# Optimization experiments

Hardware: AMD Instinct MI355X
Metric: run time of the kernel (lower is better)

## Reference

```python
import jax, jax.numpy as jnp
import numpy as np

D = 768
H = 12
DH = D // H  # 64


def setup_inputs() -> dict:
    key = jax.random.key(0)
    ks = jax.random.split(key, 7)
    B, N = 16, 1024
    sequences = jax.random.normal(ks[0], (B, N, D), dtype=jnp.float32)
    s = 1.0 / np.sqrt(DH)
    # per-head torch Linear params: weight [out, in] = [DH, DH], bias [DH]
    Wq = jax.random.uniform(ks[1], (H, DH, DH), jnp.float32, -s, s)
    Wk = jax.random.uniform(ks[2], (H, DH, DH), jnp.float32, -s, s)
    Wv = jax.random.uniform(ks[3], (H, DH, DH), jnp.float32, -s, s)
    bq = jax.random.uniform(ks[4], (H, DH), jnp.float32, -s, s)
    bk = jax.random.uniform(ks[5], (H, DH), jnp.float32, -s, s)
    bv = jax.random.uniform(ks[6], (H, DH), jnp.float32, -s, s)
    return {"sequences": sequences, "Wq": Wq, "Wk": Wk, "Wv": Wv,
            "bq": bq, "bk": bk, "bv": bv}


def reference(sequences, Wq, Wk, Wv, bq, bk, bv):
    B, N, _ = sequences.shape
    x = sequences.reshape(B, N, H, DH)  # head slices of the feature dim
    # torch Linear: y = x @ W.T + b  -> einsum over the 'in' axis of W
    q = jnp.einsum('bnhd,hed->bnhe', x, Wq) + bq
    k = jnp.einsum('bnhd,hed->bnhe', x, Wk) + bk
    v = jnp.einsum('bnhd,hed->bnhe', x, Wv) + bv
    scores = jnp.einsum('bnhe,bmhe->bhnm', q, k) / jnp.sqrt(jnp.float32(DH))
    attn = jax.nn.softmax(scores, axis=-1)  # [B,H,N,N]
    out = jnp.einsum('bhnm,bmhe->bnhe', attn, v)
    return out.reshape(B, N, H * DH)  # hstack of per-head outputs
```

## Files before the change

kernel.cpp:

```cpp
#include <hip/hip_runtime.h>


#define NH 12
#define DHEAD 64
#define BB 16
#define NSEQ 1024
#define DMODEL 768
#define LSTR 72
#define QSCALE 0.18033688f

typedef unsigned short u16;
typedef unsigned int u32;
typedef u16 u16x8 __attribute__((ext_vector_type(8)));
typedef u16 u16x4 __attribute__((ext_vector_type(4)));
typedef __bf16 bf16x8 __attribute__((ext_vector_type(8)));
typedef float f32x4 __attribute__((ext_vector_type(4)));
typedef int i32x2 __attribute__((ext_vector_type(2)));

union Frag { u16x8 u; bf16x8 b; u32 w[4]; };

__device__ __forceinline__ float fast_exp2(float x) {
#if __has_builtin(__builtin_amdgcn_exp2f)
    return __builtin_amdgcn_exp2f(x);
#else
    return exp2f(x);
#endif
}

__device__ __forceinline__ u16 f2bf(float f) {
    union { __bf16 h; u16 u; } c; c.h = (__bf16)f; return c.u;
}

__device__ __forceinline__ u32 pk2(float lo, float hi) {
    return (u32)f2bf(lo) | ((u32)f2bf(hi) << 16);
}

__device__ __forceinline__ u16x8 cvt8(const float* __restrict__ p) {
    f32x4 a = *(const f32x4*)p;
    f32x4 b = *(const f32x4*)(p + 4);
    Frag r;
    r.b[0] = (__bf16)a[0]; r.b[1] = (__bf16)a[1]; r.b[2] = (__bf16)a[2]; r.b[3] = (__bf16)a[3];
    r.b[4] = (__bf16)b[0]; r.b[5] = (__bf16)b[1]; r.b[6] = (__bf16)b[2]; r.b[7] = (__bf16)b[3];
    return r.u;
}

__device__ __forceinline__ int sw(int row, int slot) {
    return (row << 6) + (((slot + row) & 7) << 3);
}

__device__ __forceinline__ void lane4_shuffle(u32 a0, u32 a1, u32& wlo, u32& whi) {
    i32x2 t = __builtin_amdgcn_permlane32_swap((int)a0, (int)a1, false, false);
    i32x2 r = __builtin_amdgcn_permlane16_swap(t[0], t[1], false, false);
    wlo = (u32)r[0]; whi = (u32)r[1];
}

__global__ __launch_bounds__(256) void wcvt_kernel(
    const float* __restrict__ Wq, const float* __restrict__ Wk,
    const float* __restrict__ Wv, u16* __restrict__ Wb)
{
    const int bx = blockIdx.x;
    const int m = bx / 24;
    const int off = (bx % 24) * 2048 + threadIdx.x * 8;
    const float* srcs[3] = { Wq, Wk, Wv };
    *(u16x8*)(Wb + m * 49152 + off) = cvt8(srcs[m] + off);
}

__global__ __launch_bounds__(256) void kv_kernel(
    const float* __restrict__ x,
    const u16*  __restrict__ Wb,
    const float* __restrict__ bk, const float* __restrict__ bv,
    u16* __restrict__ Ko,
    u16* __restrict__ Vt)
{
    __shared__ __align__(16) u16 w_lds[2][64 * LSTR];
    __shared__ __align__(16) u16 x_lds[128 * LSTR];

    const int bid = blockIdx.x;
    const int h     = bid % NH;
    const int chunk = (bid / NH) & 7;
    const int b     = bid / (NH * 8);

    const int t = threadIdx.x, lane = t & 63, wave = t >> 6;
    const int qd = lane >> 4, lm = lane & 15;

    {
        const int row = t >> 2, d0 = (t & 3) * 16;
#pragma unroll
        for (int m = 0; m < 2; m++) {
            const u16* s = Wb + (1 + m) * 49152 + h * 4096 + row * 64 + d0;
            *(u16x8*)&w_lds[m][row * LSTR + d0]     = *(const u16x8*)s;
            *(u16x8*)&w_lds[m][row * LSTR + d0 + 8] = *(const u16x8*)(s + 8);
        }
        const int xr = t >> 1, xd = (t & 1) * 32;
        const float* s = x + ((size_t)(b * NSEQ + chunk * 128 + xr)) * DMODEL + h * DHEAD + xd;
#pragma unroll
        for (int i = 0; i < 4; i++)
            *(u16x8*)&x_lds[xr * LSTR + xd + i * 8] = cvt8(s + i * 8);
    }
    __syncthreads();

    Frag xfrag[2][2];
#pragma unroll
    for (int mt = 0; mt < 2; mt++)
#pragma unroll
        for (int kk = 0; kk < 2; kk++)
            xfrag[mt][kk].u = *(const u16x8*)&x_lds[(wave * 32 + mt * 16 + lm) * LSTR + kk * 32 + qd * 8];

    u16* tx = &x_lds[wave * 32 * LSTR];
    const int key_base = chunk * 128 + wave * 32;

#pragma unroll
    for (int et = 0; et < 4; et++) {
        Frag wfrag[2];
#pragma unroll
        for (int kk = 0; kk < 2; kk++)
            wfrag[kk].u = *(const u16x8*)&w_lds[0][(et * 16 + lm) * LSTR + kk * 32 + qd * 8];
        f32x4 acc0 = {0.f,0.f,0.f,0.f}, acc1 = {0.f,0.f,0.f,0.f};
#pragma unroll
        for (int kk = 0; kk < 2; kk++) {
            acc0 = __builtin_amdgcn_mfma_f32_16x16x32_bf16(wfrag[kk].b, xfrag[0][kk].b, acc0, 0, 0, 0);
            acc1 = __builtin_amdgcn_mfma_f32_16x16x32_bf16(wfrag[kk].b, xfrag[1][kk].b, acc1, 0, 0, 0);
        }
        f32x4 b4 = *(const f32x4*)&bk[h * DHEAD + et * 16 + qd * 4];
        u16x4 o0, o1;
#pragma unroll
        for (int r = 0; r < 4; r++) {
            o0[r] = f2bf(acc0[r] + b4[r]);
            o1[r] = f2bf(acc1[r] + b4[r]);
        }
        *(u16x4*)&tx[lm * LSTR + et * 16 + qd * 4]        = o0;
        *(u16x4*)&tx[(16 + lm) * LSTR + et * 16 + qd * 4] = o1;
    }
    {
        const size_t base_out = ((size_t)(b * NH + h) * NSEQ + key_base) * DHEAD;
#pragma unroll
        for (int j = 0; j < 4; j++) {
            const int row = j * 8 + (lane >> 3), col = (lane & 7) * 8;
            u16x8 v = *(const u16x8*)&tx[row * LSTR + col];
            *(u16x8*)(Ko + base_out + (size_t)row * DHEAD + col) = v;
        }
    }

    const size_t vt_base = ((size_t)(b * NH + h)) * DHEAD * NSEQ;
#pragma unroll
    for (int et = 0; et < 4; et++) {
        Frag wvfrag[2];
#pragma unroll
        for (int kk = 0; kk < 2; kk++)
            wvfrag[kk].u = *(const u16x8*)&w_lds[1][(et * 16 + lm) * LSTR + kk * 32 + qd * 8];
        const float bvv = bv[h * DHEAD + et * 16 + lm];
#pragma unroll
        for (int mt = 0; mt < 2; mt++) {
            f32x4 acc = {0.f,0.f,0.f,0.f};
#pragma unroll
            for (int kk = 0; kk < 2; kk++)
                acc = __builtin_amdgcn_mfma_f32_16x16x32_bf16(xfrag[mt][kk].b, wvfrag[kk].b, acc, 0, 0, 0);
            u16x4 o;
#pragma unroll
            for (int r = 0; r < 4; r++) o[r] = f2bf(acc[r] + bvv);
            *(u16x4*)(Vt + vt_base + (size_t)(et * 16 + lm) * NSEQ + key_base + mt * 16 + qd * 4) = o;
        }
    }
}

__global__ __launch_bounds__(256, 2) void attn_kernel(
    const float* __restrict__ x, const u16* __restrict__ Wb,
    const float* __restrict__ bq,
    const u16* __restrict__ K, const u16* __restrict__ Vt,
    float* __restrict__ out)
{
    __shared__ __align__(16) u16 k_lds[2][64 * 64];
    __shared__ __align__(16) u16 v_lds[2][64 * 64];

    const int bid = blockIdx.x;
    const int bh = bid % 192;
    const int qt = bid / 192;
    const int h = bh % NH, b = bh / NH;

    const int t = threadIdx.x, lane = t & 63, wave = t >> 6;
    const int qd = lane >> 4, lm = lane & 15;
    const size_t bh_off = (size_t)bh * NSEQ * DHEAD;
    const int tb = qt * 256;

    const u16* kb = K  + bh_off;
    const u16* vb = Vt + bh_off;

    const int srow = t >> 2, sc = t & 3;

    {
        const u16* wq = Wb + h * 4096 + srow * 64 + sc * 16;
        *(u16x8*)&k_lds[0][sw(srow, sc * 2)]     = *(const u16x8*)wq;
        *(u16x8*)&k_lds[0][sw(srow, sc * 2 + 1)] = *(const u16x8*)(wq + 8);
    }

    u16x8 kreg0, kreg1, vreg0, vreg1;
    {
        const u16* sk = kb + (size_t)srow * DHEAD + sc * 16;
        kreg0 = *(const u16x8*)sk; kreg1 = *(const u16x8*)(sk + 8);
        const u16* sv = vb + (size_t)srow * NSEQ + sc * 16;
        vreg0 = *(const u16x8*)sv; vreg1 = *(const u16x8*)(sv + 8);
    }
    __syncthreads();

    Frag qfrag[4][2];
#pragma unroll
    for (int mtl = 0; mtl < 4; mtl++) {
        const float* xs = x + ((size_t)(b * NSEQ + tb + wave * 64 + mtl * 16 + lm)) * DMODEL
                          + h * DHEAD + qd * 8;
        Frag xB[2];
        xB[0].u = cvt8(xs);
        xB[1].u = cvt8(xs + 32);
        u32 Ap[4], Bp[4];
#pragma unroll
        for (int et = 0; et < 4; et++) {
            Frag wqA[2];
#pragma unroll
            for (int kk = 0; kk < 2; kk++)
                wqA[kk].u = *(const u16x8*)&k_lds[0][sw(et * 16 + lm, kk * 4 + qd)];
            f32x4 acc = {0.f,0.f,0.f,0.f};
#pragma unroll
            for (int kk = 0; kk < 2; kk++)
                acc = __builtin_amdgcn_mfma_f32_16x16x32_bf16(wqA[kk].b, xB[kk].b, acc, 0, 0, 0);
            f32x4 b4 = *(const f32x4*)&bq[h * DHEAD + et * 16 + qd * 4];
            Ap[et] = pk2((acc[0] + b4[0]) * QSCALE, (acc[1] + b4[1]) * QSCALE);
            Bp[et] = pk2((acc[2] + b4[2]) * QSCALE, (acc[3] + b4[3]) * QSCALE);
        }
#pragma unroll
        for (int kk = 0; kk < 2; kk++) {
            lane4_shuffle(Ap[2 * kk], Ap[2 * kk + 1], qfrag[mtl][kk].w[0], qfrag[mtl][kk].w[2]);
            lane4_shuffle(Bp[2 * kk], Bp[2 * kk + 1], qfrag[mtl][kk].w[1], qfrag[mtl][kk].w[3]);
        }
    }

    *(u16x8*)&k_lds[1][sw(srow, sc * 2)]     = kreg0;
    *(u16x8*)&k_lds[1][sw(srow, sc * 2 + 1)] = kreg1;
    *(u16x8*)&v_lds[1][sw(srow, sc * 2)]     = vreg0;
    *(u16x8*)&v_lds[1][sw(srow, sc * 2 + 1)] = vreg1;
    {
        const u16* sk = kb + (size_t)(64 + srow) * DHEAD + sc * 16;
        kreg0 = *(const u16x8*)sk; kreg1 = *(const u16x8*)(sk + 8);
        const u16* sv = vb + (size_t)srow * NSEQ + 64 + sc * 16;
        vreg0 = *(const u16x8*)sv; vreg1 = *(const u16x8*)(sv + 8);
    }
    __syncthreads();

    f32x4 o_acc[4][4] = {};
    f32x4 rsum = {0.f, 0.f, 0.f, 0.f};

#pragma unroll 1
    for (int it = 0; it < NSEQ / 64; it++) {
        const int cur = 1 - (it & 1);

        Frag kfrag[4][2];
#pragma unroll
        for (int kt = 0; kt < 4; kt++)
#pragma unroll
            for (int kk = 0; kk < 2; kk++)
                kfrag[kt][kk].u = *(const u16x8*)&k_lds[cur][sw(kt * 16 + lm, kk * 4 + qd)];

        Frag pfrag[4][2];
#pragma unroll
        for (int mt = 0; mt < 4; mt++) {
            f32x4 st[4];
#pragma unroll
            for (int kt = 0; kt < 4; kt++) {
                f32x4 a = {0.f,0.f,0.f,0.f};
#pragma unroll
                for (int kk = 0; kk < 2; kk++)
                    a = __builtin_amdgcn_mfma_f32_16x16x32_bf16(kfrag[kt][kk].b, qfrag[mt][kk].b, a, 0, 0, 0);
                st[kt] = a;
            }
            float rs = 0.f;
            u32 Ap[4], Bp[4];
#pragma unroll
            for (int kt = 0; kt < 4; kt++) {
                float e0 = fast_exp2(st[kt][0]);
                float e1 = fast_exp2(st[kt][1]);
                float e2 = fast_exp2(st[kt][2]);
                float e3 = fast_exp2(st[kt][3]);
                rs += (e0 + e1) + (e2 + e3);
                Ap[kt] = pk2(e0, e1); Bp[kt] = pk2(e2, e3);
            }
            rsum[mt] += rs;
#pragma unroll
            for (int kk = 0; kk < 2; kk++) {
                lane4_shuffle(Ap[2 * kk], Ap[2 * kk + 1], pfrag[mt][kk].w[0], pfrag[mt][kk].w[2]);
                lane4_shuffle(Bp[2 * kk], Bp[2 * kk + 1], pfrag[mt][kk].w[1], pfrag[mt][kk].w[3]);
            }
        }

#pragma unroll
        for (int dt = 0; dt < 4; dt++) {
            Frag vfrag[2];
#pragma unroll
            for (int kk = 0; kk < 2; kk++)
                vfrag[kk].u = *(const u16x8*)&v_lds[cur][sw(dt * 16 + lm, kk * 4 + qd)];
#pragma unroll
            for (int kk = 0; kk < 2; kk++)
#pragma unroll
                for (int mt = 0; mt < 4; mt++)
                    o_acc[mt][dt] = __builtin_amdgcn_mfma_f32_16x16x32_bf16(pfrag[mt][kk].b, vfrag[kk].b, o_acc[mt][dt], 0, 0, 0);
        }

        if (it < NSEQ / 64 - 1) {
            *(u16x8*)&k_lds[1 - cur][sw(srow, sc * 2)]     = kreg0;
            *(u16x8*)&k_lds[1 - cur][sw(srow, sc * 2 + 1)] = kreg1;
            *(u16x8*)&v_lds[1 - cur][sw(srow, sc * 2)]     = vreg0;
            *(u16x8*)&v_lds[1 - cur][sw(srow, sc * 2 + 1)] = vreg1;
        }
        if (it < NSEQ / 64 - 2) {
            const u16* sk = kb + (size_t)((it + 2) * 64 + srow) * DHEAD + sc * 16;
            kreg0 = *(const u16x8*)sk; kreg1 = *(const u16x8*)(sk + 8);
            const u16* sv = vb + (size_t)srow * NSEQ + (it + 2) * 64 + sc * 16;
            vreg0 = *(const u16x8*)sv; vreg1 = *(const u16x8*)(sv + 8);
        }
        __syncthreads();
    }

#pragma unroll
    for (int mt = 0; mt < 4; mt++) {
        float s = rsum[mt];
        s += __shfl_xor(s, 16);
        s += __shfl_xor(s, 32);
        float inv = 1.f / s;
        float inv4[4];
#pragma unroll
        for (int r = 0; r < 4; r++) inv4[r] = __shfl(inv, qd * 4 + r);
#pragma unroll
        for (int dt = 0; dt < 4; dt++) {
            const int e = dt * 16 + lm;
#pragma unroll
            for (int r = 0; r < 4; r++) {
                const int n_tok = tb + wave * 64 + mt * 16 + qd * 4 + r;
                out[((size_t)(b * NSEQ + n_tok)) * DMODEL + h * DHEAD + e] =
                    o_acc[mt][dt][r] * inv4[r];
            }
        }
    }
}

extern "C" void kernel_launch(void* const* d_in, const int* in_sizes, int n_in,
                              void* d_out, int out_size, void* d_ws, size_t ws_size,
                              hipStream_t stream) {
    const float* x  = (const float*)d_in[0];
    const float* Wq = (const float*)d_in[1];
    const float* Wk = (const float*)d_in[2];
    const float* Wv = (const float*)d_in[3];
    const float* bq = (const float*)d_in[4];
    const float* bk = (const float*)d_in[5];
    const float* bv = (const float*)d_in[6];
    float* out = (float*)d_out;

    const size_t KV_ELEMS = (size_t)BB * NH * NSEQ * DHEAD;
    u16* Kw  = (u16*)d_ws;
    u16* Vtw = Kw + KV_ELEMS;
    u16* Wb  = Vtw + KV_ELEMS;

    wcvt_kernel<<<72, 256, 0, stream>>>(Wq, Wk, Wv, Wb);
    kv_kernel<<<BB * 8 * NH, 256, 0, stream>>>(x, Wb, bk, bv, Kw, Vtw);
    attn_kernel<<<(NSEQ / 256) * BB * NH, 256, 0, stream>>>(x, Wb, bq, Kw, Vtw, out);
}
```

Measured before the change: 99.13 us.

## Software-pipeline QK and PV MFMAs per query tile with setprio and higher occupancy

Restructures the attention inner loop so the QK^T scores for the next query sub-tile are issued while the exp/pack/shuffle of the current one runs, and the PV MFMAs are applied per sub-tile instead of after all four. V fragments are hoisted to registers once per iteration, and s_setprio raises wave priority around MFMA bursts. It also raises launch bounds to 3 blocks per CU and uses a packed bf16x2 conversion. The aim is to overlap transcendental/VALU work with matrix-core work. The cost is more live registers under a tighter occupancy bound, which risks spilling.

```diff
diff --git a/kernel.cpp b/kernel.cpp
--- a/kernel.cpp
+++ b/kernel.cpp
@@ -14,6 +14,7 @@
 typedef u16 u16x8 __attribute__((ext_vector_type(8)));
 typedef u16 u16x4 __attribute__((ext_vector_type(4)));
 typedef __bf16 bf16x8 __attribute__((ext_vector_type(8)));
+typedef __bf16 bf16x2 __attribute__((ext_vector_type(2)));
 typedef float f32x4 __attribute__((ext_vector_type(4)));
 typedef int i32x2 __attribute__((ext_vector_type(2)));
 
@@ -32,7 +33,9 @@
 }
 
 __device__ __forceinline__ u32 pk2(float lo, float hi) {
-    return (u32)f2bf(lo) | ((u32)f2bf(hi) << 16);
+    union { bf16x2 b; u32 u; } c;
+    c.b[0] = (__bf16)lo; c.b[1] = (__bf16)hi;
+    return c.u;
 }
 
 __device__ __forceinline__ u16x8 cvt8(const float* __restrict__ p) {
@@ -163,7 +166,7 @@
     }
 }
 
-__global__ __launch_bounds__(256, 2) void attn_kernel(
+__global__ __launch_bounds__(256, 3) void attn_kernel(
     const float* __restrict__ x, const u16* __restrict__ Wb,
     const float* __restrict__ bq,
     const u16* __restrict__ K, const u16* __restrict__ Vt,
@@ -257,19 +260,39 @@
 #pragma unroll
             for (int kk = 0; kk < 2; kk++)
                 kfrag[kt][kk].u = *(const u16x8*)&k_lds[cur][sw(kt * 16 + lm, kk * 4 + qd)];
-
-        Frag pfrag[4][2];
+        Frag vfrag[4][2];
+#pragma unroll
+        for (int dt = 0; dt < 4; dt++)
+#pragma unroll
+            for (int kk = 0; kk < 2; kk++)
+                vfrag[dt][kk].u = *(const u16x8*)&v_lds[cur][sw(dt * 16 + lm, kk * 4 + qd)];
+
+        f32x4 st[4];
+        __builtin_amdgcn_s_setprio(1);
+#pragma unroll
+        for (int kt = 0; kt < 4; kt++) {
+            f32x4 a = {0.f,0.f,0.f,0.f};
+            a = __builtin_amdgcn_mfma_f32_16x16x32_bf16(kfrag[kt][0].b, qfrag[0][0].b, a, 0, 0, 0);
+            a = __builtin_amdgcn_mfma_f32_16x16x32_bf16(kfrag[kt][1].b, qfrag[0][1].b, a, 0, 0, 0);
+            st[kt] = a;
+        }
+        __builtin_amdgcn_s_setprio(0);
+
 #pragma unroll
         for (int mt = 0; mt < 4; mt++) {
-            f32x4 st[4];
-#pragma unroll
-            for (int kt = 0; kt < 4; kt++) {
-                f32x4 a = {0.f,0.f,0.f,0.f};
-#pragma unroll
-                for (int kk = 0; kk < 2; kk++)
-                    a = __builtin_amdgcn_mfma_f32_16x16x32_bf16(kfrag[kt][kk].b, qfrag[mt][kk].b, a, 0, 0, 0);
-                st[kt] = a;
-            }
+            f32x4 stn[4];
+            if (mt < 3) {
+                __builtin_amdgcn_s_setprio(1);
+#pragma unroll
+                for (int kt = 0; kt < 4; kt++) {
+                    f32x4 a = {0.f,0.f,0.f,0.f};
+                    a = __builtin_amdgcn_mfma_f32_16x16x32_bf16(kfrag[kt][0].b, qfrag[mt + 1][0].b, a, 0, 0, 0);
+                    a = __builtin_amdgcn_mfma_f32_16x16x32_bf16(kfrag[kt][1].b, qfrag[mt + 1][1].b, a, 0, 0, 0);
+                    stn[kt] = a;
+                }
+                __builtin_amdgcn_s_setprio(0);
+            }
+
             float rs = 0.f;
             u32 Ap[4], Bp[4];
 #pragma unroll
@@ -282,24 +305,25 @@
                 Ap[kt] = pk2(e0, e1); Bp[kt] = pk2(e2, e3);
             }
             rsum[mt] += rs;
+            Frag pfrag[2];
 #pragma unroll
             for (int kk = 0; kk < 2; kk++) {
-                lane4_shuffle(Ap[2 * kk], Ap[2 * kk + 1], pfrag[mt][kk].w[0], pfrag[mt][kk].w[2]);
-                lane4_shuffle(Bp[2 * kk], Bp[2 * kk + 1], pfrag[mt][kk].w[1], pfrag[mt][kk].w[3]);
-            }
-        }
-
-#pragma unroll
-        for (int dt = 0; dt < 4; dt++) {
-            Frag vfrag[2];
-#pragma unroll
-            for (int kk = 0; kk < 2; kk++)
-                vfrag[kk].u = *(const u16x8*)&v_lds[cur][sw(dt * 16 + lm, kk * 4 + qd)];
-#pragma unroll
-            for (int kk = 0; kk < 2; kk++)
-#pragma unroll
-                for (int mt = 0; mt < 4; mt++)
-                    o_acc[mt][dt] = __builtin_amdgcn_mfma_f32_16x16x32_bf16(pfrag[mt][kk].b, vfrag[kk].b, o_acc[mt][dt], 0, 0, 0);
+                lane4_shuffle(Ap[2 * kk], Ap[2 * kk + 1], pfrag[kk].w[0], pfrag[kk].w[2]);
+                lane4_shuffle(Bp[2 * kk], Bp[2 * kk + 1], pfrag[kk].w[1], pfrag[kk].w[3]);
+            }
+
+            __builtin_amdgcn_s_setprio(1);
+#pragma unroll
+            for (int dt = 0; dt < 4; dt++)
+#pragma unroll
+                for (int kk = 0; kk < 2; kk++)
+                    o_acc[mt][dt] = __builtin_amdgcn_mfma_f32_16x16x32_bf16(pfrag[kk].b, vfrag[dt][kk].b, o_acc[mt][dt], 0, 0, 0);
+            __builtin_amdgcn_s_setprio(0);
+
+            if (mt < 3) {
+#pragma unroll
+                for (int kt = 0; kt < 4; kt++) st[kt] = stn[kt];
+            }
         }
 
         if (it < NSEQ / 64 - 1) {
```

Result: slower. 332.8 us (+235.7%).

## Load K/V fragments directly from global memory, dropping LDS double buffering

Applied to the files above, without the earlier changes.

The attention loop now reads K and transposed-V MFMA fragments straight from global memory into registers instead of staging them through double-buffered shared memory. This removes the per-iteration LDS writes and the block-wide __syncthreads, and shrinks shared memory to the Wq tile only. The cost is that each of the four waves fetches the same K/V tiles separately, relying on L1/L2 for reuse, and global load latency is no longer hidden by an explicit prefetch. The bf16 pair-packing helper is also rewritten to use a vector bf16x2 conversion.

```diff
diff --git a/kernel.cpp b/kernel.cpp
--- a/kernel.cpp
+++ b/kernel.cpp
@@ -14,6 +14,7 @@
 typedef u16 u16x8 __attribute__((ext_vector_type(8)));
 typedef u16 u16x4 __attribute__((ext_vector_type(4)));
 typedef __bf16 bf16x8 __attribute__((ext_vector_type(8)));
+typedef __bf16 bf16x2 __attribute__((ext_vector_type(2)));
 typedef float f32x4 __attribute__((ext_vector_type(4)));
 typedef int i32x2 __attribute__((ext_vector_type(2)));
 
@@ -32,7 +33,9 @@
 }
 
 __device__ __forceinline__ u32 pk2(float lo, float hi) {
-    return (u32)f2bf(lo) | ((u32)f2bf(hi) << 16);
+    union { bf16x2 b; u32 u; } c;
+    c.b[0] = (__bf16)lo; c.b[1] = (__bf16)hi;
+    return c.u;
 }
 
 __device__ __forceinline__ u16x8 cvt8(const float* __restrict__ p) {
@@ -169,8 +172,7 @@
     const u16* __restrict__ K, const u16* __restrict__ Vt,
     float* __restrict__ out)
 {
-    __shared__ __align__(16) u16 k_lds[2][64 * 64];
-    __shared__ __align__(16) u16 v_lds[2][64 * 64];
+    __shared__ __align__(16) u16 wq_lds[64 * 64];
 
     const int bid = blockIdx.x;
     const int bh = bid % 192;
@@ -185,20 +187,11 @@
     const u16* kb = K  + bh_off;
     const u16* vb = Vt + bh_off;
 
-    const int srow = t >> 2, sc = t & 3;
-
     {
+        const int srow = t >> 2, sc = t & 3;
         const u16* wq = Wb + h * 4096 + srow * 64 + sc * 16;
-        *(u16x8*)&k_lds[0][sw(srow, sc * 2)]     = *(const u16x8*)wq;
-        *(u16x8*)&k_lds[0][sw(srow, sc * 2 + 1)] = *(const u16x8*)(wq + 8);
-    }
-
-    u16x8 kreg0, kreg1, vreg0, vreg1;
-    {
-        const u16* sk = kb + (size_t)srow * DHEAD + sc * 16;
-        kreg0 = *(const u16x8*)sk; kreg1 = *(const u16x8*)(sk + 8);
-        const u16* sv = vb + (size_t)srow * NSEQ + sc * 16;
-        vreg0 = *(const u16x8*)sv; vreg1 = *(const u16x8*)(sv + 8);
+        *(u16x8*)&wq_lds[sw(srow, sc * 2)]     = *(const u16x8*)wq;
+        *(u16x8*)&wq_lds[sw(srow, sc * 2 + 1)] = *(const u16x8*)(wq + 8);
     }
     __syncthreads();
 
@@ -216,7 +209,7 @@
             Frag wqA[2];
 #pragma unroll
             for (int kk = 0; kk < 2; kk++)
-                wqA[kk].u = *(const u16x8*)&k_lds[0][sw(et * 16 + lm, kk * 4 + qd)];
+                wqA[kk].u = *(const u16x8*)&wq_lds[sw(et * 16 + lm, kk * 4 + qd)];
             f32x4 acc = {0.f,0.f,0.f,0.f};
 #pragma unroll
             for (int kk = 0; kk < 2; kk++)
@@ -232,31 +225,30 @@
         }
     }
 
-    *(u16x8*)&k_lds[1][sw(srow, sc * 2)]     = kreg0;
-    *(u16x8*)&k_lds[1][sw(srow, sc * 2 + 1)] = kreg1;
-    *(u16x8*)&v_lds[1][sw(srow, sc * 2)]     = vreg0;
-    *(u16x8*)&v_lds[1][sw(srow, sc * 2 + 1)] = vreg1;
-    {
-        const u16* sk = kb + (size_t)(64 + srow) * DHEAD + sc * 16;
-        kreg0 = *(const u16x8*)sk; kreg1 = *(const u16x8*)(sk + 8);
-        const u16* sv = vb + (size_t)srow * NSEQ + 64 + sc * 16;
-        vreg0 = *(const u16x8*)sv; vreg1 = *(const u16x8*)(sv + 8);
-    }
-    __syncthreads();
-
     f32x4 o_acc[4][4] = {};
     f32x4 rsum = {0.f, 0.f, 0.f, 0.f};
 
+    const int k_off = lm * DHEAD + qd * 8;
+    const int v_off = lm * NSEQ + qd * 8;
+
 #pragma unroll 1
     for (int it = 0; it < NSEQ / 64; it++) {
-        const int cur = 1 - (it & 1);
+        const u16* kt0 = kb + it * (64 * DHEAD);
+        const u16* vt0 = vb + it * 64;
 
         Frag kfrag[4][2];
 #pragma unroll
         for (int kt = 0; kt < 4; kt++)
 #pragma unroll
             for (int kk = 0; kk < 2; kk++)
-                kfrag[kt][kk].u = *(const u16x8*)&k_lds[cur][sw(kt * 16 + lm, kk * 4 + qd)];
+                kfrag[kt][kk].u = *(const u16x8*)(kt0 + kt * (16 * DHEAD) + kk * 32 + k_off);
+
+        Frag vfrag[4][2];
+#pragma unroll
+        for (int dt = 0; dt < 4; dt++)
+#pragma unroll
+            for (int kk = 0; kk < 2; kk++)
+                vfrag[dt][kk].u = *(const u16x8*)(vt0 + dt * (16 * NSEQ) + kk * 32 + v_off);
 
         Frag pfrag[4][2];
 #pragma unroll
@@ -290,31 +282,12 @@
         }
 
 #pragma unroll
-        for (int dt = 0; dt < 4; dt++) {
-            Frag vfrag[2];
-#pragma unroll
-            for (int kk = 0; kk < 2; kk++)
-                vfrag[kk].u = *(const u16x8*)&v_lds[cur][sw(dt * 16 + lm, kk * 4 + qd)];
+        for (int dt = 0; dt < 4; dt++)
 #pragma unroll
             for (int kk = 0; kk < 2; kk++)
 #pragma unroll
                 for (int mt = 0; mt < 4; mt++)
-                    o_acc[mt][dt] = __builtin_amdgcn_mfma_f32_16x16x32_bf16(pfrag[mt][kk].b, vfrag[kk].b, o_acc[mt][dt], 0, 0, 0);
-        }
-
-        if (it < NSEQ / 64 - 1) {
-            *(u16x8*)&k_lds[1 - cur][sw(srow, sc * 2)]     = kreg0;
-            *(u16x8*)&k_lds[1 - cur][sw(srow, sc * 2 + 1)] = kreg1;
-            *(u16x8*)&v_lds[1 - cur][sw(srow, sc * 2)]     = vreg0;
-            *(u16x8*)&v_lds[1 - cur][sw(srow, sc * 2 + 1)] = vreg1;
-        }
-        if (it < NSEQ / 64 - 2) {
-            const u16* sk = kb + (size_t)((it + 2) * 64 + srow) * DHEAD + sc * 16;
-            kreg0 = *(const u16x8*)sk; kreg1 = *(const u16x8*)(sk + 8);
-            const u16* sv = vb + (size_t)srow * NSEQ + (it + 2) * 64 + sc * 16;
-            vreg0 = *(const u16x8*)sv; vreg1 = *(const u16x8*)(sv + 8);
-        }
-        __syncthreads();
+                    o_acc[mt][dt] = __builtin_amdgcn_mfma_f32_16x16x32_bf16(pfrag[mt][kk].b, vfrag[dt][kk].b, o_acc[mt][dt], 0, 0, 0);
     }
 
 #pragma unroll
```

New measurement: 136.7 us. 37.9% more time.
